# Kernel tuning notes

Hardware: AMD Instinct MI355X
Metric: run time of the kernel (lower is better)

The kernel has to match this reference:

```python
import jax, jax.numpy as jnp
import numpy as np


def quaternion_to_matrix(q):
    # pytorch3d convention: real-first (r, i, j, k); handles unnormalized quats
    r, i, j, k = q[..., 0], q[..., 1], q[..., 2], q[..., 3]
    two_s = 2.0 / jnp.sum(q * q, axis=-1)
    o = jnp.stack([
        1 - two_s * (j * j + k * k), two_s * (i * j - k * r), two_s * (i * k + j * r),
        two_s * (i * j + k * r), 1 - two_s * (i * i + k * k), two_s * (j * k - i * r),
        two_s * (i * k - j * r), two_s * (j * k + i * r), 1 - two_s * (i * i + j * j),
    ], axis=-1)
    return o.reshape(q.shape[:-1] + (3, 3))


def setup_inputs() -> dict:
    key = jax.random.key(0)
    ks = jax.random.split(key, 6)
    B, N = 32, 120000
    predT = jax.random.normal(ks[0], (B, 7), dtype=jnp.float32)
    ptCldT = 10.0 * jax.random.normal(ks[1], (B, N, 4), dtype=jnp.float32)
    targetTransformT = jax.random.normal(ks[2], (B, 4, 4), dtype=jnp.float32)
    # calib matrices: near-identity so R_rect @ RT is well-conditioned for inverse
    R_rect = jnp.eye(4, dtype=jnp.float32) + 0.05 * jax.random.normal(ks[3], (4, 4), dtype=jnp.float32)
    RT = jnp.eye(4, dtype=jnp.float32) + 0.05 * jax.random.normal(ks[4], (4, 4), dtype=jnp.float32)
    ptCldSize = jax.random.randint(ks[5], (B,), 1, N + 1, dtype=jnp.int32)
    return {"predT": predT, "ptCldT": ptCldT, "targetTransformT": targetTransformT,
            "R_rect": R_rect, "RT": RT, "ptCldSize": ptCldSize}


def reference(predT, ptCldT, targetTransformT, R_rect, RT, ptCldSize):
    B, N = ptCldT.shape[0], ptCldT.shape[1]
    predRot = quaternion_to_matrix(predT[:, :4])          # [B,3,3]
    predTrans = predT[:, 4:]                              # [B,3]
    gtR = targetTransformT[:, :3, :3]
    gtT = targetTransformT[:, :3, 3]

    # rotation loss: ||R_pred^T @ R_gt - I||_F per batch (vectorized over B)
    M = jnp.einsum('bji,bjk->bik', predRot, gtR)
    eye3 = jnp.eye(3, dtype=M.dtype)
    rotationLoss = jnp.sqrt(jnp.sum((M - eye3) ** 2, axis=(1, 2)))   # [B]

    # translation loss: ||t_pred - t_gt||_2 per batch
    translationLoss = jnp.sqrt(jnp.sum((predTrans - gtT) ** 2, axis=-1))  # [B]

    # ground-truth base point cloud: undo rectification + extrinsics
    ones = jnp.ones((B, N, 1), dtype=ptCldT.dtype)
    homo = jnp.concatenate([ptCldT[..., :3], ones], axis=-1)  # [B,N,4]
    invCalib = jnp.linalg.inv(R_rect @ RT)                    # [4,4]
    base = jnp.einsum('ij,bnj->bni', invCalib, homo)          # [B,N,4]
    baseHomo = jnp.concatenate([base[..., :3], ones], axis=-1)

    # SE3 from predicted rotation + translation
    top = jnp.concatenate([predRot, predTrans[:, :, None]], axis=2)  # [B,3,4]
    bottom = jnp.broadcast_to(jnp.array([0.0, 0.0, 0.0, 1.0], dtype=top.dtype), (B, 1, 4))
    predSE3 = jnp.concatenate([top, bottom], axis=1)                  # [B,4,4]

    ptTarget = jnp.einsum('bij,bnj->bni', targetTransformT, baseHomo)
    ptPred = jnp.einsum('bij,bnj->bni', predSE3, baseHomo)

    # per-point euclidean distance, masked mean over valid points per batch
    dist = jnp.sqrt(jnp.sum((ptTarget[..., :3] - ptPred[..., :3]) ** 2, axis=-1))  # [B,N]
    mask = (jnp.arange(N)[None, :] < ptCldSize[:, None]).astype(dist.dtype)
    perBatch = jnp.sum(dist * mask, axis=1) / jnp.maximum(ptCldSize, 1).astype(dist.dtype)

    eucl = jnp.mean(perBatch)
    totalLoss = eucl + 1.5 * jnp.mean(translationLoss) + 2.0 * jnp.mean(rotationLoss)
    return totalLoss.astype(jnp.float32), eucl
```

## Files before the change

### kernel.cpp

```cpp
#include <hip/hip_runtime.h>
#include <math.h>

#define PB  64
#define TPB 256


__global__ void prep_kernel(const float* __restrict__ predT,
                            const float* __restrict__ target,
                            const float* __restrict__ R_rect,
                            const float* __restrict__ RT,
                            float* __restrict__ ws, int B)
{
    __shared__ float invC[16];
    int tid = threadIdx.x;
    if (tid == 0) {
        float a[4][8];
        for (int i = 0; i < 4; ++i)
            for (int j = 0; j < 4; ++j) {
                float s = 0.f;
                for (int k = 0; k < 4; ++k) s += R_rect[i*4+k] * RT[k*4+j];
                a[i][j]   = s;
                a[i][j+4] = (i == j) ? 1.f : 0.f;
            }
        for (int col = 0; col < 4; ++col) {
            int p = col; float best = fabsf(a[col][col]);
            for (int r = col+1; r < 4; ++r) {
                float v = fabsf(a[r][col]);
                if (v > best) { best = v; p = r; }
            }
            if (p != col)
                for (int j = 0; j < 8; ++j) { float t = a[col][j]; a[col][j] = a[p][j]; a[p][j] = t; }
            float inv = 1.f / a[col][col];
            for (int j = 0; j < 8; ++j) a[col][j] *= inv;
            for (int r = 0; r < 4; ++r) if (r != col) {
                float f = a[r][col];
                for (int j = 0; j < 8; ++j) a[r][j] -= f * a[col][j];
            }
        }
        for (int i = 0; i < 4; ++i)
            for (int j = 0; j < 4; ++j)
                invC[i*4+j] = a[i][j+4];
    }
    __syncthreads();

    float rl_acc = 0.f, tl_acc = 0.f;
    for (int b = tid; b < B; b += blockDim.x) {
        const float* q = predT + b*7;
        float r = q[0], qi = q[1], qj = q[2], qk = q[3];
        float tx = q[4], ty = q[5], tz = q[6];
        float s = 2.f / (r*r + qi*qi + qj*qj + qk*qk);
        float R[3][3];
        R[0][0] = 1.f - s*(qj*qj + qk*qk); R[0][1] = s*(qi*qj - qk*r);       R[0][2] = s*(qi*qk + qj*r);
        R[1][0] = s*(qi*qj + qk*r);       R[1][1] = 1.f - s*(qi*qi + qk*qk); R[1][2] = s*(qj*qk - qi*r);
        R[2][0] = s*(qi*qk - qj*r);       R[2][1] = s*(qj*qk + qi*r);       R[2][2] = 1.f - s*(qi*qi + qj*qj);

        const float* T = target + b*16;

        float rl = 0.f;
        for (int i = 0; i < 3; ++i)
            for (int k = 0; k < 3; ++k) {
                float m = R[0][i]*T[0*4+k] + R[1][i]*T[1*4+k] + R[2][i]*T[2*4+k];
                m -= (i == k) ? 1.f : 0.f;
                rl += m*m;
            }
        rl_acc += sqrtf(rl);

        float dx = tx - T[3], dy = ty - T[7], dz = tz - T[11];
        tl_acc += sqrtf(dx*dx + dy*dy + dz*dz);

        float tr[3] = {tx, ty, tz};
        float D[3][4];
        for (int i = 0; i < 3; ++i) {
            for (int j = 0; j < 3; ++j) D[i][j] = T[i*4+j] - R[i][j];
            D[i][3] = T[i*4+3] - tr[i];
        }
        float* o = ws + b*12;
        for (int i = 0; i < 3; ++i) {
            for (int k = 0; k < 3; ++k)
                o[i*3+k] = D[i][0]*invC[0*4+k] + D[i][1]*invC[1*4+k] + D[i][2]*invC[2*4+k];
            o[9+i]    = D[i][0]*invC[3]     + D[i][1]*invC[7]     + D[i][2]*invC[11]    + D[i][3];
        }
    }
    for (int off = 32; off > 0; off >>= 1) {
        rl_acc += __shfl_down(rl_acc, off);
        tl_acc += __shfl_down(tl_acc, off);
    }
    if (tid == 0)
        ws[B*12 + B*PB] = 1.5f * (tl_acc / (float)B) + 2.0f * (rl_acc / (float)B);
}

__global__ __launch_bounds__(TPB) void dist_kernel(
    const float4* __restrict__ pts, const int* __restrict__ sizes,
    const float* __restrict__ ws, float* __restrict__ partials, int N)
{
    int b = blockIdx.y;
    const float* m = ws + b*12;
    float m00=m[0], m01=m[1], m02=m[2];
    float m10=m[3], m11=m[4], m12=m[5];
    float m20=m[6], m21=m[7], m22=m[8];
    float t0=m[9], t1=m[10], t2=m[11];
    int size = sizes[b];
    const float4* p = pts + (size_t)b * N;

    float acc = 0.f;
    for (int n = blockIdx.x * TPB + threadIdx.x; n < size; n += PB * TPB) {
        float4 v = p[n];
        float dx = m00*v.x + m01*v.y + m02*v.z + t0;
        float dy = m10*v.x + m11*v.y + m12*v.z + t1;
        float dz = m20*v.x + m21*v.y + m22*v.z + t2;
        acc += sqrtf(dx*dx + dy*dy + dz*dz);
    }

    __shared__ float sm[TPB/64];
    for (int off = 32; off > 0; off >>= 1) acc += __shfl_down(acc, off);
    if ((threadIdx.x & 63) == 0) sm[threadIdx.x >> 6] = acc;
    __syncthreads();
    if (threadIdx.x == 0) {
        float s = 0.f;
        for (int w = 0; w < TPB/64; ++w) s += sm[w];
        partials[b * PB + blockIdx.x] = s;
    }
}

__global__ void final_kernel(const float* __restrict__ partials,
                             const int* __restrict__ sizes,
                             const float* __restrict__ scalar_part,
                             float* __restrict__ out, int B)
{
    int tid = threadIdx.x;
    float acc = 0.f;
    for (int b = tid; b < B; b += 64) {
        float s = 0.f;
        for (int i = 0; i < PB; ++i) s += partials[b*PB + i];
        int sz = sizes[b];
        acc += s / (float)(sz > 1 ? sz : 1);
    }
    for (int off = 32; off > 0; off >>= 1) acc += __shfl_down(acc, off);
    if (tid == 0) {
        float eucl = acc / (float)B;
        out[0] = eucl + scalar_part[0];
        out[1] = eucl;
    }
}

extern "C" void kernel_launch(void* const* d_in, const int* in_sizes, int n_in,
                              void* d_out, int out_size, void* d_ws, size_t ws_size,
                              hipStream_t stream) {
    const float* predT  = (const float*)d_in[0];
    const float* ptCld  = (const float*)d_in[1];
    const float* target = (const float*)d_in[2];
    const float* R_rect = (const float*)d_in[3];
    const float* RT     = (const float*)d_in[4];
    const int*   sizes  = (const int*)d_in[5];

    int B = in_sizes[0] / 7;
    int N = in_sizes[1] / (B * 4);

    float* ws       = (float*)d_ws;
    float* partials = ws + B*12;
    float* scal     = ws + B*12 + B*PB;
    float* out      = (float*)d_out;

    prep_kernel<<<1, 64, 0, stream>>>(predT, target, R_rect, RT, ws, B);
    dist_kernel<<<dim3(PB, B), TPB, 0, stream>>>((const float4*)ptCld, sizes, ws, partials, N);
    final_kernel<<<1, 64, 0, stream>>>(partials, sizes, scal, out, B);
}
```

Baseline: 18.21 us.

## Fuse prep, distance and final reduction into one kernel with last-block reduction

Merges the three launches into a single kernel. Each block recomputes the 4x4 calibration inverse and its batch's combined transform in thread 0. The last block, found through an atomic counter, does the final reduction and the rotation and translation losses. This removes two kernel launches and the dependency gaps between them, at the cost of redundant per-block serial prep work and a memset for the counter. B is hardcoded to 32 in the last-block check.

```diff
diff --git a/kernel.cpp b/kernel.cpp
--- a/kernel.cpp
+++ b/kernel.cpp
@@ -3,16 +3,29 @@
 
 #define PB  64
 #define TPB 256
+#define B_  32
 
 
-__global__ void prep_kernel(const float* __restrict__ predT,
-                            const float* __restrict__ target,
-                            const float* __restrict__ R_rect,
-                            const float* __restrict__ RT,
-                            float* __restrict__ ws, int B)
+__global__ __launch_bounds__(TPB) void fused_kernel(
+    const float* __restrict__ predT,
+    const float4* __restrict__ pts,
+    const float* __restrict__ target,
+    const float* __restrict__ R_rect,
+    const float* __restrict__ RT,
+    const int* __restrict__ sizes,
+    float* __restrict__ partials,
+    unsigned* __restrict__ counter,
+    float* __restrict__ out,
+    int N)
 {
-    __shared__ float invC[16];
-    int tid = threadIdx.x;
+    const int b   = blockIdx.y;
+    const int blk = blockIdx.x;
+    const int tid = threadIdx.x;
+
+    __shared__ float sM[12];
+    __shared__ float sm[TPB/64];
+    __shared__ bool  isLast;
+
     if (tid == 0) {
         float a[4][8];
         for (int i = 0; i < 4; ++i)
@@ -37,73 +50,40 @@
                 for (int j = 0; j < 8; ++j) a[r][j] -= f * a[col][j];
             }
         }
-        for (int i = 0; i < 4; ++i)
-            for (int j = 0; j < 4; ++j)
-                invC[i*4+j] = a[i][j+4];
-    }
-    __syncthreads();
-
-    float rl_acc = 0.f, tl_acc = 0.f;
-    for (int b = tid; b < B; b += blockDim.x) {
         const float* q = predT + b*7;
         float r = q[0], qi = q[1], qj = q[2], qk = q[3];
         float tx = q[4], ty = q[5], tz = q[6];
-        float s = 2.f / (r*r + qi*qi + qj*qj + qk*qk);
+        float s2 = 2.f / (r*r + qi*qi + qj*qj + qk*qk);
         float R[3][3];
-        R[0][0] = 1.f - s*(qj*qj + qk*qk); R[0][1] = s*(qi*qj - qk*r);       R[0][2] = s*(qi*qk + qj*r);
-        R[1][0] = s*(qi*qj + qk*r);       R[1][1] = 1.f - s*(qi*qi + qk*qk); R[1][2] = s*(qj*qk - qi*r);
-        R[2][0] = s*(qi*qk - qj*r);       R[2][1] = s*(qj*qk + qi*r);       R[2][2] = 1.f - s*(qi*qi + qj*qj);
+        R[0][0] = 1.f - s2*(qj*qj + qk*qk); R[0][1] = s2*(qi*qj - qk*r);        R[0][2] = s2*(qi*qk + qj*r);
+        R[1][0] = s2*(qi*qj + qk*r);        R[1][1] = 1.f - s2*(qi*qi + qk*qk); R[1][2] = s2*(qj*qk - qi*r);
+        R[2][0] = s2*(qi*qk - qj*r);        R[2][1] = s2*(qj*qk + qi*r);        R[2][2] = 1.f - s2*(qi*qi + qj*qj);
 
         const float* T = target + b*16;
-
-        float rl = 0.f;
-        for (int i = 0; i < 3; ++i)
-            for (int k = 0; k < 3; ++k) {
-                float m = R[0][i]*T[0*4+k] + R[1][i]*T[1*4+k] + R[2][i]*T[2*4+k];
-                m -= (i == k) ? 1.f : 0.f;
-                rl += m*m;
-            }
-        rl_acc += sqrtf(rl);
-
-        float dx = tx - T[3], dy = ty - T[7], dz = tz - T[11];
-        tl_acc += sqrtf(dx*dx + dy*dy + dz*dz);
-
         float tr[3] = {tx, ty, tz};
         float D[3][4];
         for (int i = 0; i < 3; ++i) {
             for (int j = 0; j < 3; ++j) D[i][j] = T[i*4+j] - R[i][j];
             D[i][3] = T[i*4+3] - tr[i];
         }
-        float* o = ws + b*12;
         for (int i = 0; i < 3; ++i) {
             for (int k = 0; k < 3; ++k)
-                o[i*3+k] = D[i][0]*invC[0*4+k] + D[i][1]*invC[1*4+k] + D[i][2]*invC[2*4+k];
-            o[9+i]    = D[i][0]*invC[3]     + D[i][1]*invC[7]     + D[i][2]*invC[11]    + D[i][3];
+                sM[i*3+k] = D[i][0]*a[0][4+k] + D[i][1]*a[1][4+k] + D[i][2]*a[2][4+k];
+            sM[9+i]     = D[i][0]*a[0][7]    + D[i][1]*a[1][7]    + D[i][2]*a[2][7]    + D[i][3];
         }
     }
-    for (int off = 32; off > 0; off >>= 1) {
-        rl_acc += __shfl_down(rl_acc, off);
-        tl_acc += __shfl_down(tl_acc, off);
-    }
-    if (tid == 0)
-        ws[B*12 + B*PB] = 1.5f * (tl_acc / (float)B) + 2.0f * (rl_acc / (float)B);
-}
+    __syncthreads();
 
-__global__ __launch_bounds__(TPB) void dist_kernel(
-    const float4* __restrict__ pts, const int* __restrict__ sizes,
-    const float* __restrict__ ws, float* __restrict__ partials, int N)
-{
-    int b = blockIdx.y;
-    const float* m = ws + b*12;
-    float m00=m[0], m01=m[1], m02=m[2];
-    float m10=m[3], m11=m[4], m12=m[5];
-    float m20=m[6], m21=m[7], m22=m[8];
-    float t0=m[9], t1=m[10], t2=m[11];
-    int size = sizes[b];
+    const float m00=sM[0], m01=sM[1], m02=sM[2];
+    const float m10=sM[3], m11=sM[4], m12=sM[5];
+    const float m20=sM[6], m21=sM[7], m22=sM[8];
+    const float t0=sM[9], t1=sM[10], t2=sM[11];
+
+    const int size = sizes[b];
     const float4* p = pts + (size_t)b * N;
 
     float acc = 0.f;
-    for (int n = blockIdx.x * TPB + threadIdx.x; n < size; n += PB * TPB) {
+    for (int n = blk * TPB + tid; n < size; n += PB * TPB) {
         float4 v = p[n];
         float dx = m00*v.x + m01*v.y + m02*v.z + t0;
         float dy = m10*v.x + m11*v.y + m12*v.z + t1;
@@ -111,35 +91,73 @@
         acc += sqrtf(dx*dx + dy*dy + dz*dz);
     }
 
-    __shared__ float sm[TPB/64];
     for (int off = 32; off > 0; off >>= 1) acc += __shfl_down(acc, off);
-    if ((threadIdx.x & 63) == 0) sm[threadIdx.x >> 6] = acc;
+    if ((tid & 63) == 0) sm[tid >> 6] = acc;
     __syncthreads();
-    if (threadIdx.x == 0) {
+    if (tid == 0) {
         float s = 0.f;
         for (int w = 0; w < TPB/64; ++w) s += sm[w];
-        partials[b * PB + blockIdx.x] = s;
+        partials[b * PB + blk] = s;
+        __threadfence();
+        unsigned old = atomicAdd(counter, 1u);
+        isLast = (old == (unsigned)(PB * B_ - 1));
     }
-}
+    __syncthreads();
+    if (!isLast) return;
 
-__global__ void final_kernel(const float* __restrict__ partials,
-                             const int* __restrict__ sizes,
-                             const float* __restrict__ scalar_part,
-                             float* __restrict__ out, int B)
-{
-    int tid = threadIdx.x;
-    float acc = 0.f;
-    for (int b = tid; b < B; b += 64) {
+    __threadfence();
+
+    __shared__ float sB[B_];
+    {
+        int bb = tid >> 3, j = tid & 7;
         float s = 0.f;
-        for (int i = 0; i < PB; ++i) s += partials[b*PB + i];
-        int sz = sizes[b];
-        acc += s / (float)(sz > 1 ? sz : 1);
+        const float* pp = partials + bb * PB + j * 8;
+        #pragma unroll
+        for (int i = 0; i < 8; ++i) s += pp[i];
+        s += __shfl_down(s, 4);
+        s += __shfl_down(s, 2);
+        s += __shfl_down(s, 1);
+        if (j == 0) {
+            int sz = sizes[bb];
+            sB[bb] = s / (float)(sz > 1 ? sz : 1);
+        }
     }
-    for (int off = 32; off > 0; off >>= 1) acc += __shfl_down(acc, off);
-    if (tid == 0) {
-        float eucl = acc / (float)B;
-        out[0] = eucl + scalar_part[0];
-        out[1] = eucl;
+    __syncthreads();
+
+    if (tid < 64) {
+        float accE = 0.f, accT = 0.f, accR = 0.f;
+        if (tid < B_) {
+            accE = sB[tid];
+            const float* q = predT + tid*7;
+            float r = q[0], qi = q[1], qj = q[2], qk = q[3];
+            float tx = q[4], ty = q[5], tz = q[6];
+            float s2 = 2.f / (r*r + qi*qi + qj*qj + qk*qk);
+            float R[3][3];
+            R[0][0] = 1.f - s2*(qj*qj + qk*qk); R[0][1] = s2*(qi*qj - qk*r);        R[0][2] = s2*(qi*qk + qj*r);
+            R[1][0] = s2*(qi*qj + qk*r);        R[1][1] = 1.f - s2*(qi*qi + qk*qk); R[1][2] = s2*(qj*qk - qi*r);
+            R[2][0] = s2*(qi*qk - qj*r);        R[2][1] = s2*(qj*qk + qi*r);        R[2][2] = 1.f - s2*(qi*qi + qj*qj);
+            const float* T = target + tid*16;
+            float rl = 0.f;
+            for (int i = 0; i < 3; ++i)
+                for (int k = 0; k < 3; ++k) {
+                    float m = R[0][i]*T[0*4+k] + R[1][i]*T[1*4+k] + R[2][i]*T[2*4+k];
+                    m -= (i == k) ? 1.f : 0.f;
+                    rl += m*m;
+                }
+            accR = sqrtf(rl);
+            float dx = tx - T[3], dy = ty - T[7], dz = tz - T[11];
+            accT = sqrtf(dx*dx + dy*dy + dz*dz);
+        }
+        for (int off = 32; off > 0; off >>= 1) {
+            accE += __shfl_down(accE, off);
+            accT += __shfl_down(accT, off);
+            accR += __shfl_down(accR, off);
+        }
+        if (tid == 0) {
+            float eucl = accE / (float)B_;
+            out[0] = eucl + 1.5f * (accT / (float)B_) + 2.0f * (accR / (float)B_);
+            out[1] = eucl;
+        }
     }
 }
 
@@ -156,12 +174,12 @@
     int B = in_sizes[0] / 7;
     int N = in_sizes[1] / (B * 4);
 
-    float* ws       = (float*)d_ws;
-    float* partials = ws + B*12;
-    float* scal     = ws + B*12 + B*PB;
-    float* out      = (float*)d_out;
+    float*    partials = (float*)d_ws;
+    unsigned* counter  = (unsigned*)(partials + B * PB);
+    float*    out      = (float*)d_out;
 
-    prep_kernel<<<1, 64, 0, stream>>>(predT, target, R_rect, RT, ws, B);
-    dist_kernel<<<dim3(PB, B), TPB, 0, stream>>>((const float4*)ptCld, sizes, ws, partials, N);
-    final_kernel<<<1, 64, 0, stream>>>(partials, sizes, scal, out, B);
+    hipMemsetAsync(counter, 0, sizeof(unsigned), stream);
+    fused_kernel<<<dim3(PB, B), TPB, 0, stream>>>(
+        predT, (const float4*)ptCld, target, R_rect, RT, sizes,
+        partials, counter, out, N);
 }
```

After: 68.07 us. 3.74x slower.
